# Optimization experiments

Measured on AMD Instinct MI355X. Metric: run time of the kernel, lower is better.

The kernel has to match this reference:

```python
import jax, jax.numpy as jnp
import numpy as np


def setup_inputs() -> dict:
    key = jax.random.key(0)
    k1, k2, k3, k4 = jax.random.split(key, 4)
    B, Sq, Sk, d = 16, 2048, 2048, 64
    queries = jax.random.normal(k1, (B, Sq, d), dtype=jnp.float32)
    keys = jax.random.normal(k2, (B, Sk, d), dtype=jnp.float32)
    values = jax.random.normal(k3, (B, Sk, d), dtype=jnp.float32)
    # True = padded key position (masked out)
    key_padding_mask = jax.random.randint(k4, (B, Sk), 0, 2) == 1
    return {"queries": queries, "keys": keys, "values": values,
            "key_padding_mask": key_padding_mask}


def reference(queries, keys, values, key_padding_mask):
    d = queries.shape[-1]
    # scores: [B, Sq, Sk]
    scores = jnp.einsum("bqd,bkd->bqk", queries, keys) / jnp.sqrt(
        jnp.asarray(d, dtype=queries.dtype))
    # padded keys get -inf before softmax (mask broadcast over query dim)
    scores = jnp.where(key_padding_mask[:, None, :], -jnp.inf, scores)
    attention_weights = jax.nn.softmax(scores, axis=2)
    return jnp.einsum("bqk,bkd->bqd", attention_weights, values)
```

## Files before the change

### kernel.cpp

```cpp
#include <hip/hip_runtime.h>
#include <hip/hip_bf16.h>

#define NB 16
#define SQ 2048
#define SK 2048
#define DH 64

#define KBLK 1024
#define VBLK 512
#define BBLK 128

typedef __attribute__((ext_vector_type(8))) short short8;
typedef __attribute__((ext_vector_type(8))) __bf16 bf16x8;
typedef __attribute__((ext_vector_type(4))) float floatx4;
typedef __attribute__((ext_vector_type(16))) float floatx16;
typedef __attribute__((ext_vector_type(2))) unsigned uint2v;

#define GLOB const __attribute__((address_space(1))) void*
#define LDSP __attribute__((address_space(3))) void*

__device__ __forceinline__ unsigned pk2(float a, float b) {
  __hip_bfloat162 h = __float22bfloat162_rn(make_float2(a, b));
  unsigned u; __builtin_memcpy(&u, &h, 4); return u;
}
__device__ __forceinline__ floatx16 mfma32(short8 a, short8 b, floatx16 c) {
  return __builtin_amdgcn_mfma_f32_32x32x16_bf16(
      __builtin_bit_cast(bf16x8, a), __builtin_bit_cast(bf16x8, b), c, 0, 0, 0);
}

__device__ __forceinline__ int swap23(int k) {
  return (((k >> 2) ^ (k >> 3)) & 1) ? (k ^ 12) : k;
}

__global__ __launch_bounds__(256)
void prepass(const float* __restrict__ K, const float* __restrict__ V,
             const int* __restrict__ m, short* __restrict__ Kb,
             short* __restrict__ Vt, float* __restrict__ bias) {
  __shared__ unsigned tlw[64 * 33];
  const int blk = blockIdx.x;
  const int t = threadIdx.x;
  if (blk < KBLK) {
    size_t i8 = ((size_t)blk * 256 + t) * 8;
    floatx4 a = *(const floatx4*)(K + i8);
    floatx4 b = *(const floatx4*)(K + i8 + 4);
    union { unsigned u[4]; short8 s; } w;
    w.u[0] = pk2(a[0], a[1]); w.u[1] = pk2(a[2], a[3]);
    w.u[2] = pk2(b[0], b[1]); w.u[3] = pk2(b[2], b[3]);
    const int local = (int)(i8 & 4095);
    const int key = local >> 6, chunk = (local >> 3) & 7;
    const int prow = swap23(key);
    const size_t tb = i8 & ~(size_t)4095;
    *(short8*)(Kb + tb + prow * 64 + ((chunk ^ (prow & 7)) << 3)) = w.s;
  } else if (blk < KBLK + VBLK) {
    const int bt = blk - KBLK;
    const int key2 = t & 31;
    const int dg = (t >> 5) * 8;
    const float* vp0 = V + ((size_t)bt * 64 + 2 * key2) * 64 + dg;
    const float* vp1 = vp0 + 64;
    floatx4 va  = *(const floatx4*)(vp0);
    floatx4 va2 = *(const floatx4*)(vp0 + 4);
    floatx4 vb  = *(const floatx4*)(vp1);
    floatx4 vb2 = *(const floatx4*)(vp1 + 4);
#pragma unroll
    for (int j = 0; j < 4; ++j) {
      tlw[(dg + j) * 33 + key2]     = pk2(va[j],  vb[j]);
      tlw[(dg + 4 + j) * 33 + key2] = pk2(va2[j], vb2[j]);
    }
    __syncthreads();
    const short* tls = (const short*)tlw;
    short* dst = Vt + (size_t)bt * 4096;
#pragma unroll
    for (int i = 0; i < 2; ++i) {
      int idx = i * 2048 + t * 8;
      int d = idx >> 6, key = idx & 63;
      int chunk = key >> 3;
      *(short8*)(dst + d * 64 + ((chunk ^ (d & 7)) << 3)) =
          *(const short8*)(tls + d * 66 + key);
    }
  } else {
    int i = (blk - KBLK - VBLK) * 256 + t;
    bias[i] = m[i] ? -1e30f : 0.0f;
  }
}

__global__ __launch_bounds__(256, 1)
void attn_main(const float* __restrict__ Q, const short* __restrict__ Kb,
               const short* __restrict__ Vt, const float* __restrict__ bias,
               float* __restrict__ Out) {
  __shared__ __align__(16) short ks[2][4096];
  __shared__ __align__(16) short vt[2][4096];
  __shared__ __align__(16) float bsh[2048];

  const int gid = blockIdx.x;
  const int xcd = gid & 7;
  const int j   = gid >> 3;
  const int b   = xcd + 8 * (j >> 4);
  const int qt  = j & 15;
  const int tid  = threadIdx.x;
  const int wave = tid >> 6;
  const int lane = tid & 63;
  const int n32  = lane & 31;
  const int h    = lane >> 5;
  const int sw   = n32 & 7;
  const int q0   = qt * 128 + wave * 32;

  const float QS = 0.125f * 1.4426950408889634f;
  short8 qf[4];
  {
    const float* qp = Q + ((size_t)b * SQ + q0 + n32) * DH + 8 * h;
#pragma unroll
    for (int c = 0; c < 4; ++c) {
      floatx4 a  = *(const floatx4*)(qp + 16 * c);
      floatx4 a2 = *(const floatx4*)(qp + 16 * c + 4);
      union { unsigned u[4]; short8 s; } w;
      w.u[0] = pk2(a[0] * QS, a[1] * QS);
      w.u[1] = pk2(a[2] * QS, a[3] * QS);
      w.u[2] = pk2(a2[0] * QS, a2[1] * QS);
      w.u[3] = pk2(a2[2] * QS, a2[3] * QS);
      qf[c] = w.s;
    }
  }

  {
    const float* bp = bias + (size_t)b * SK + tid * 8;
    *(floatx4*)(bsh + tid * 8)     = *(const floatx4*)(bp);
    *(floatx4*)(bsh + tid * 8 + 4) = *(const floatx4*)(bp + 4);
  }

  floatx16 o0, o1;
#pragma unroll
  for (int i = 0; i < 16; ++i) { o0[i] = 0.f; o1[i] = 0.f; }
  float l_q = 0.f;

  const short* kg = Kb + (size_t)b * SK * DH;
  const short* vg = Vt + (size_t)b * 32 * 4096;

  const int lo0 = (wave * 2) * 512;
  const int lo1 = (wave * 2 + 1) * 512;
  const int go0 = lo0 + lane * 8;
  const int go1 = lo1 + lane * 8;

#define ISSUE_K(tile, buf) do {                                                        \
    const short* kn_ = kg + (size_t)(tile) * 4096;                                     \
    __builtin_amdgcn_global_load_lds((GLOB)(kn_ + go0), (LDSP)&ks[buf][lo0], 16, 0, 0);\
    __builtin_amdgcn_global_load_lds((GLOB)(kn_ + go1), (LDSP)&ks[buf][lo1], 16, 0, 0);\
  } while (0)
#define ISSUE_V(tile, buf) do {                                                        \
    const short* vn_ = vg + (size_t)(tile) * 4096;                                     \
    __builtin_amdgcn_global_load_lds((GLOB)(vn_ + go0), (LDSP)&vt[buf][lo0], 16, 0, 0);\
    __builtin_amdgcn_global_load_lds((GLOB)(vn_ + go1), (LDSP)&vt[buf][lo1], 16, 0, 0);\
  } while (0)

  floatx16 sA[2], sB[2];

#define QK(tt, d) do {                                                                 \
    const float* bq_ = bsh + (tt) * 64 + 8 * h;                                        \
    _Pragma("unroll") for (int u = 0; u < 4; ++u) {                                    \
      const int off_ = 16 * (u >> 1) + 4 * (u & 1);                                    \
      floatx4 bv0_ = *(const floatx4*)(bq_ + off_);                                    \
      floatx4 bv1_ = *(const floatx4*)(bq_ + 32 + off_);                               \
      _Pragma("unroll") for (int i = 0; i < 4; ++i) {                                  \
        sA[d][4 * u + i] = bv0_[i]; sB[d][4 * u + i] = bv1_[i]; } }                    \
    _Pragma("unroll") for (int c = 0; c < 4; ++c) {                                    \
      short8 kf0_ = *(short8*)(ks[(tt) & 1] + n32 * 64        + ((2 * c + h) ^ sw) * 8);\
      short8 kf1_ = *(short8*)(ks[(tt) & 1] + (32 + n32) * 64 + ((2 * c + h) ^ sw) * 8);\
      sA[d] = mfma32(kf0_, qf[c], sA[d]);                                              \
      sB[d] = mfma32(kf1_, qf[c], sB[d]); }                                            \
  } while (0)

  asm volatile("s_waitcnt vmcnt(0) lgkmcnt(0)" ::: "memory");
  __builtin_amdgcn_sched_barrier(0);
  ISSUE_K(0, 0); ISSUE_V(0, 0); ISSUE_K(1, 1); ISSUE_V(1, 1);
  asm volatile("s_waitcnt vmcnt(6)" ::: "memory");
  __builtin_amdgcn_s_barrier();
  __builtin_amdgcn_sched_barrier(0);
  QK(0, 0);

#pragma unroll 2
  for (int t = 0; t < 32; ++t) {
    if (t < 31) asm volatile("s_waitcnt vmcnt(2)" ::: "memory");
    else        asm volatile("s_waitcnt vmcnt(0)" ::: "memory");
    __builtin_amdgcn_s_barrier();
    __builtin_amdgcn_sched_barrier(0);

    if (t < 30) ISSUE_K(t + 2, t & 1);

    uint2v pka[4], pkb[4];
    {
      float rs = 0.f;
#pragma unroll
      for (int u = 0; u < 4; ++u) {
        float p0 = __builtin_amdgcn_exp2f(sA[t & 1][4 * u + 0]);
        float p1 = __builtin_amdgcn_exp2f(sA[t & 1][4 * u + 1]);
        float p2 = __builtin_amdgcn_exp2f(sA[t & 1][4 * u + 2]);
        float p3 = __builtin_amdgcn_exp2f(sA[t & 1][4 * u + 3]);
        float r0 = __builtin_amdgcn_exp2f(sB[t & 1][4 * u + 0]);
        float r1 = __builtin_amdgcn_exp2f(sB[t & 1][4 * u + 1]);
        float r2 = __builtin_amdgcn_exp2f(sB[t & 1][4 * u + 2]);
        float r3 = __builtin_amdgcn_exp2f(sB[t & 1][4 * u + 3]);
        rs += ((p0 + p1) + (p2 + p3)) + ((r0 + r1) + (r2 + r3));
        pka[u].x = pk2(p0, p1); pka[u].y = pk2(p2, p3);
        pkb[u].x = pk2(r0, r1); pkb[u].y = pk2(r2, r3);
      }
      l_q += rs;
    }
    if (t < 31) QK(t + 1, (t + 1) & 1);

#pragma unroll
    for (int c = 0; c < 4; ++c) {
      const uint2v* X = (c < 2) ? pka : pkb;
      union { unsigned u[4]; short8 s; } pf;
      pf.u[0] = X[2 * (c & 1)].x;     pf.u[1] = X[2 * (c & 1)].y;
      pf.u[2] = X[2 * (c & 1) + 1].x; pf.u[3] = X[2 * (c & 1) + 1].y;
      short8 vf0 = *(short8*)(vt[t & 1] + n32 * 64        + ((2 * c + h) ^ sw) * 8);
      short8 vf1 = *(short8*)(vt[t & 1] + (32 + n32) * 64 + ((2 * c + h) ^ sw) * 8);
      o0 = mfma32(vf0, pf.s, o0);
      o1 = mfma32(vf1, pf.s, o1);
    }

    if (t < 30) {
      __builtin_amdgcn_s_barrier();
      __builtin_amdgcn_sched_barrier(0);
      ISSUE_V(t + 2, t & 1);
    }
  }
#undef ISSUE_K
#undef ISSUE_V
#undef QK

  l_q += __shfl_xor(l_q, 32);
  const float inv = 1.0f / l_q;

  float* orow = Out + ((size_t)b * SQ + q0 + n32) * DH;
#pragma unroll
  for (int u = 0; u < 4; ++u) {
    floatx4 w0, w1;
#pragma unroll
    for (int i = 0; i < 4; ++i) { w0[i] = o0[4 * u + i] * inv; w1[i] = o1[4 * u + i] * inv; }
    *(floatx4*)(orow + 8 * u + 4 * h)      = w0;
    *(floatx4*)(orow + 32 + 8 * u + 4 * h) = w1;
  }
}

extern "C" void kernel_launch(void* const* d_in, const int* in_sizes, int n_in,
                              void* d_out, int out_size, void* d_ws, size_t ws_size,
                              hipStream_t stream) {
  const float* Q = (const float*)d_in[0];
  const float* K = (const float*)d_in[1];
  const float* V = (const float*)d_in[2];
  const int* mask = (const int*)d_in[3];
  float* Out = (float*)d_out;

  char* ws = (char*)d_ws;
  short* Kb   = (short*)(ws);
  short* Vt   = (short*)(ws + 4194304);
  float* bias = (float*)(ws + 8388608);

  prepass  <<<KBLK + VBLK + BBLK, 256, 0, stream>>>(K, V, mask, Kb, Vt, bias);
  attn_main<<<NB * (SQ / 128), 256, 0, stream>>>(Q, Kb, Vt, bias, Out);
}
```

Before: 111.3 us.

## Split key range across wave pairs and reduce partial outputs through LDS

Each block now covers 64 queries instead of 128. Its four waves form two pairs, and each pair processes half of the key tiles, so the grid doubles to 512 blocks and launch bounds allow two blocks per CU. At the end the two halves' partial outputs and row sums are combined through shared memory before normalisation. MFMA sections are also wrapped in s_setprio raises. The aim is more parallelism and latency hiding, at the cost of double the LDS buffers, an extra reduction with barriers, and each wave loading more data per tile.

```diff
diff --git a/kernel.cpp b/kernel.cpp
--- a/kernel.cpp
+++ b/kernel.cpp
@@ -9,6 +9,8 @@
 #define KBLK 1024
 #define VBLK 512
 #define BBLK 128
+
+#define NT 16
 
 typedef __attribute__((ext_vector_type(8))) short short8;
 typedef __attribute__((ext_vector_type(8))) __bf16 bf16x8;
@@ -83,26 +85,29 @@
   }
 }
 
-__global__ __launch_bounds__(256, 1)
+__global__ __launch_bounds__(256, 2)
 void attn_main(const float* __restrict__ Q, const short* __restrict__ Kb,
                const short* __restrict__ Vt, const float* __restrict__ bias,
                float* __restrict__ Out) {
-  __shared__ __align__(16) short ks[2][4096];
-  __shared__ __align__(16) short vt[2][4096];
+  __shared__ __align__(16) short ksp[2][2][4096];
+  __shared__ __align__(16) short vtp[2][2][4096];
   __shared__ __align__(16) float bsh[2048];
 
   const int gid = blockIdx.x;
   const int xcd = gid & 7;
   const int j   = gid >> 3;
-  const int b   = xcd + 8 * (j >> 4);
-  const int qt  = j & 15;
+  const int b   = xcd + 8 * (j >> 5);
+  const int qt  = j & 31;
   const int tid  = threadIdx.x;
   const int wave = tid >> 6;
   const int lane = tid & 63;
+  const int wp   = wave & 1;
+  const int pr   = wave >> 1;
   const int n32  = lane & 31;
   const int h    = lane >> 5;
   const int sw   = n32 & 7;
-  const int q0   = qt * 128 + wave * 32;
+  const int q0   = qt * 64 + wp * 32;
+  const int kt0  = pr * NT;
 
   const float QS = 0.125f * 1.4426950408889634f;
   short8 qf[4];
@@ -132,58 +137,61 @@
   for (int i = 0; i < 16; ++i) { o0[i] = 0.f; o1[i] = 0.f; }
   float l_q = 0.f;
 
-  const short* kg = Kb + (size_t)b * SK * DH;
-  const short* vg = Vt + (size_t)b * 32 * 4096;
-
-  const int lo0 = (wave * 2) * 512;
-  const int lo1 = (wave * 2 + 1) * 512;
-  const int go0 = lo0 + lane * 8;
-  const int go1 = lo1 + lane * 8;
-
-#define ISSUE_K(tile, buf) do {                                                        \
-    const short* kn_ = kg + (size_t)(tile) * 4096;                                     \
-    __builtin_amdgcn_global_load_lds((GLOB)(kn_ + go0), (LDSP)&ks[buf][lo0], 16, 0, 0);\
-    __builtin_amdgcn_global_load_lds((GLOB)(kn_ + go1), (LDSP)&ks[buf][lo1], 16, 0, 0);\
+  const short* kg = Kb + ((size_t)b * SK + (size_t)kt0 * 64) * DH;
+  const short* vg = Vt + ((size_t)b * 32 + kt0) * 4096;
+
+#define ISSUE_K(tile, buf) do {                                                          \
+    const short* kn_ = kg + (size_t)(tile) * 4096 + wp * 2048;                           \
+    short* ld_ = &ksp[pr][buf][wp * 2048];                                               \
+    __builtin_amdgcn_global_load_lds((GLOB)(kn_ + lane * 8),        (LDSP)(ld_),        16, 0, 0);\
+    __builtin_amdgcn_global_load_lds((GLOB)(kn_ + 512 + lane * 8),  (LDSP)(ld_ + 512),  16, 0, 0);\
+    __builtin_amdgcn_global_load_lds((GLOB)(kn_ + 1024 + lane * 8), (LDSP)(ld_ + 1024), 16, 0, 0);\
+    __builtin_amdgcn_global_load_lds((GLOB)(kn_ + 1536 + lane * 8), (LDSP)(ld_ + 1536), 16, 0, 0);\
   } while (0)
-#define ISSUE_V(tile, buf) do {                                                        \
-    const short* vn_ = vg + (size_t)(tile) * 4096;                                     \
-    __builtin_amdgcn_global_load_lds((GLOB)(vn_ + go0), (LDSP)&vt[buf][lo0], 16, 0, 0);\
-    __builtin_amdgcn_global_load_lds((GLOB)(vn_ + go1), (LDSP)&vt[buf][lo1], 16, 0, 0);\
+#define ISSUE_V(tile, buf) do {                                                          \
+    const short* vn_ = vg + (size_t)(tile) * 4096 + wp * 2048;                           \
+    short* ld_ = &vtp[pr][buf][wp * 2048];                                               \
+    __builtin_amdgcn_global_load_lds((GLOB)(vn_ + lane * 8),        (LDSP)(ld_),        16, 0, 0);\
+    __builtin_amdgcn_global_load_lds((GLOB)(vn_ + 512 + lane * 8),  (LDSP)(ld_ + 512),  16, 0, 0);\
+    __builtin_amdgcn_global_load_lds((GLOB)(vn_ + 1024 + lane * 8), (LDSP)(ld_ + 1024), 16, 0, 0);\
+    __builtin_amdgcn_global_load_lds((GLOB)(vn_ + 1536 + lane * 8), (LDSP)(ld_ + 1536), 16, 0, 0);\
   } while (0)
 
   floatx16 sA[2], sB[2];
 
-#define QK(tt, d) do {                                                                 \
-    const float* bq_ = bsh + (tt) * 64 + 8 * h;                                        \
-    _Pragma("unroll") for (int u = 0; u < 4; ++u) {                                    \
-      const int off_ = 16 * (u >> 1) + 4 * (u & 1);                                    \
-      floatx4 bv0_ = *(const floatx4*)(bq_ + off_);                                    \
-      floatx4 bv1_ = *(const floatx4*)(bq_ + 32 + off_);                               \
-      _Pragma("unroll") for (int i = 0; i < 4; ++i) {                                  \
-        sA[d][4 * u + i] = bv0_[i]; sB[d][4 * u + i] = bv1_[i]; } }                    \
-    _Pragma("unroll") for (int c = 0; c < 4; ++c) {                                    \
-      short8 kf0_ = *(short8*)(ks[(tt) & 1] + n32 * 64        + ((2 * c + h) ^ sw) * 8);\
-      short8 kf1_ = *(short8*)(ks[(tt) & 1] + (32 + n32) * 64 + ((2 * c + h) ^ sw) * 8);\
-      sA[d] = mfma32(kf0_, qf[c], sA[d]);                                              \
-      sB[d] = mfma32(kf1_, qf[c], sB[d]); }                                            \
+#define QK(tt, d) do {                                                                   \
+    const float* bq_ = bsh + (kt0 + (tt)) * 64 + 8 * h;                                  \
+    _Pragma("unroll") for (int u = 0; u < 4; ++u) {                                      \
+      const int off_ = 16 * (u >> 1) + 4 * (u & 1);                                      \
+      floatx4 bv0_ = *(const floatx4*)(bq_ + off_);                                      \
+      floatx4 bv1_ = *(const floatx4*)(bq_ + 32 + off_);                                 \
+      _Pragma("unroll") for (int i = 0; i < 4; ++i) {                                    \
+        sA[d][4 * u + i] = bv0_[i]; sB[d][4 * u + i] = bv1_[i]; } }                      \
+    __builtin_amdgcn_s_setprio(1);                                                       \
+    _Pragma("unroll") for (int c = 0; c < 4; ++c) {                                      \
+      short8 kf0_ = *(short8*)(ksp[pr][(tt) & 1] + n32 * 64        + ((2 * c + h) ^ sw) * 8);\
+      short8 kf1_ = *(short8*)(ksp[pr][(tt) & 1] + (32 + n32) * 64 + ((2 * c + h) ^ sw) * 8);\
+      sA[d] = mfma32(kf0_, qf[c], sA[d]);                                                \
+      sB[d] = mfma32(kf1_, qf[c], sB[d]); }                                              \
+    __builtin_amdgcn_s_setprio(0);                                                       \
   } while (0)
 
   asm volatile("s_waitcnt vmcnt(0) lgkmcnt(0)" ::: "memory");
   __builtin_amdgcn_sched_barrier(0);
   ISSUE_K(0, 0); ISSUE_V(0, 0); ISSUE_K(1, 1); ISSUE_V(1, 1);
-  asm volatile("s_waitcnt vmcnt(6)" ::: "memory");
+  asm volatile("s_waitcnt vmcnt(12)" ::: "memory");
   __builtin_amdgcn_s_barrier();
   __builtin_amdgcn_sched_barrier(0);
   QK(0, 0);
 
 #pragma unroll 2
-  for (int t = 0; t < 32; ++t) {
-    if (t < 31) asm volatile("s_waitcnt vmcnt(2)" ::: "memory");
-    else        asm volatile("s_waitcnt vmcnt(0)" ::: "memory");
+  for (int t = 0; t < NT; ++t) {
+    if (t < NT - 1) asm volatile("s_waitcnt vmcnt(4)" ::: "memory");
+    else            asm volatile("s_waitcnt vmcnt(0)" ::: "memory");
     __builtin_amdgcn_s_barrier();
     __builtin_amdgcn_sched_barrier(0);
 
-    if (t < 30) ISSUE_K(t + 2, t & 1);
+    if (t < NT - 2) ISSUE_K(t + 2, t & 1);
 
     uint2v pka[4], pkb[4];
     {
@@ -204,21 +212,23 @@
       }
       l_q += rs;
     }
-    if (t < 31) QK(t + 1, (t + 1) & 1);
-
+    if (t < NT - 1) QK(t + 1, (t + 1) & 1);
+
+    __builtin_amdgcn_s_setprio(1);
 #pragma unroll
     for (int c = 0; c < 4; ++c) {
       const uint2v* X = (c < 2) ? pka : pkb;
       union { unsigned u[4]; short8 s; } pf;
       pf.u[0] = X[2 * (c & 1)].x;     pf.u[1] = X[2 * (c & 1)].y;
       pf.u[2] = X[2 * (c & 1) + 1].x; pf.u[3] = X[2 * (c & 1) + 1].y;
-      short8 vf0 = *(short8*)(vt[t & 1] + n32 * 64        + ((2 * c + h) ^ sw) * 8);
-      short8 vf1 = *(short8*)(vt[t & 1] + (32 + n32) * 64 + ((2 * c + h) ^ sw) * 8);
+      short8 vf0 = *(short8*)(vtp[pr][t & 1] + n32 * 64        + ((2 * c + h) ^ sw) * 8);
+      short8 vf1 = *(short8*)(vtp[pr][t & 1] + (32 + n32) * 64 + ((2 * c + h) ^ sw) * 8);
       o0 = mfma32(vf0, pf.s, o0);
       o1 = mfma32(vf1, pf.s, o1);
     }
-
-    if (t < 30) {
+    __builtin_amdgcn_s_setprio(0);
+
+    if (t < NT - 2) {
       __builtin_amdgcn_s_barrier();
       __builtin_amdgcn_sched_barrier(0);
       ISSUE_V(t + 2, t & 1);
@@ -229,16 +239,35 @@
 #undef QK
 
   l_q += __shfl_xor(l_q, 32);
-  const float inv = 1.0f / l_q;
-
-  float* orow = Out + ((size_t)b * SQ + q0 + n32) * DH;
-#pragma unroll
-  for (int u = 0; u < 4; ++u) {
-    floatx4 w0, w1;
-#pragma unroll
-    for (int i = 0; i < 4; ++i) { w0[i] = o0[4 * u + i] * inv; w1[i] = o1[4 * u + i] * inv; }
-    *(floatx4*)(orow + 8 * u + 4 * h)      = w0;
-    *(floatx4*)(orow + 32 + 8 * u + 4 * h) = w1;
+
+  __syncthreads();
+  float* Xs = (float*)&ksp[0][0][0];
+  float* Ls = (float*)&vtp[0][0][0];
+  if (pr == 1) {
+#pragma unroll
+    for (int e = 0; e < 16; ++e) {
+      Xs[e * 128 + wp * 64 + lane]        = o0[e];
+      Xs[(16 + e) * 128 + wp * 64 + lane] = o1[e];
+    }
+    Ls[wp * 64 + lane] = l_q;
+  }
+  __syncthreads();
+  if (pr == 0) {
+#pragma unroll
+    for (int e = 0; e < 16; ++e) {
+      o0[e] += Xs[e * 128 + wp * 64 + lane];
+      o1[e] += Xs[(16 + e) * 128 + wp * 64 + lane];
+    }
+    const float inv = 1.0f / (l_q + Ls[wp * 64 + lane]);
+    float* orow = Out + ((size_t)b * SQ + q0 + n32) * DH;
+#pragma unroll
+    for (int u = 0; u < 4; ++u) {
+      floatx4 w0, w1;
+#pragma unroll
+      for (int i = 0; i < 4; ++i) { w0[i] = o0[4 * u + i] * inv; w1[i] = o1[4 * u + i] * inv; }
+      *(floatx4*)(orow + 8 * u + 4 * h)      = w0;
+      *(floatx4*)(orow + 32 + 8 * u + 4 * h) = w1;
+    }
   }
 }
 
@@ -257,5 +286,5 @@
   float* bias = (float*)(ws + 8388608);
 
   prepass  <<<KBLK + VBLK + BBLK, 256, 0, stream>>>(K, V, mask, Kb, Vt, bias);
-  attn_main<<<NB * (SQ / 128), 256, 0, stream>>>(Q, Kb, Vt, bias, Out);
-}
+  attn_main<<<NB * (SQ / 64), 256, 0, stream>>>(Q, Kb, Vt, bias, Out);
+}
```

After: 104.5 us. 6.1% less time.
